# Optimization experiments

Measured on AMD Instinct MI355X. Metric: run time of the kernel, lower is better.

## Reference

```python
import jax, jax.numpy as jnp
import numpy as np

B, S, C = 8, 2048, 1024

def setup_inputs() -> dict:
    key = jax.random.key(0)
    ks = jax.random.split(key, 9)
    scale = 1.0 / np.sqrt(C)
    return {
        "x1": jax.random.normal(ks[0], (B, S, C), jnp.float32),
        "x2": jax.random.normal(ks[1], (B, S, C), jnp.float32),
        "x3": jax.random.normal(ks[2], (B, S, C), jnp.float32),
        "Wq": jax.random.normal(ks[3], (C, C), jnp.float32) * scale,
        "bq": jax.random.normal(ks[4], (C,), jnp.float32) * scale,
        "Wk": jax.random.normal(ks[5], (C, C), jnp.float32) * scale,
        "bk": jax.random.normal(ks[6], (C,), jnp.float32) * scale,
        "Wv": jax.random.normal(ks[7], (C, C), jnp.float32) * scale,
        "bv": jax.random.normal(ks[8], (C,), jnp.float32) * scale,
    }

def reference(x1, x2, x3, Wq, bq, Wk, bk, Wv, bv):
    # Linear layers: x @ W^T + b (torch nn.Linear convention, W is [out, in])
    q = jnp.einsum('bsc,dc->bsd', x1, Wq) + bq  # [B,S,C]
    k = jnp.einsum('bsc,dc->bsd', x2, Wk) + bk
    v = jnp.einsum('bsc,dc->bsd', x3, Wv) + bv
    # NOTE: original has NO 1/sqrt(d) scaling
    scores = jnp.einsum('bqd,bkd->bqk', q, k)   # [B,S,S]
    attn = jax.nn.softmax(scores, axis=-1)
    return jnp.einsum('bqk,bkd->bqd', attn, v)  # [B,S,C]
```

## Files before the change

kernel.cpp:

```cpp
#include <hip/hip_runtime.h>
#include <stdint.h>

namespace {

constexpr int Bn = 8;
constexpr int Sn = 2048;
constexpr int Cn = 1024;
constexpr int Mn = Bn * Sn;

typedef float f32x4 __attribute__((ext_vector_type(4)));
typedef _Float16 f16x8 __attribute__((ext_vector_type(8)));
typedef unsigned short us8 __attribute__((ext_vector_type(8)));

__device__ __forceinline__ unsigned short f2h(float f) {
  _Float16 h = (_Float16)f;
  unsigned short u;
  __builtin_memcpy(&u, &h, 2);
  return u;
}

__device__ __forceinline__ void stage16(const unsigned short* g, unsigned short* l) {
  __builtin_amdgcn_global_load_lds(
      (const __attribute__((address_space(1))) void*)g,
      (__attribute__((address_space(3))) void*)l, 16, 0, 0);
}

__global__ __launch_bounds__(256) void k_cast16(const float* __restrict__ src,
                                                unsigned short* __restrict__ dst, int n) {
  int stride = gridDim.x * blockDim.x;
  for (int i = blockIdx.x * blockDim.x + threadIdx.x; i * 4 < n; i += stride) {
    int j = i * 4;
    float4 v = *(const float4*)(src + j);
    ushort4 h;
    h.x = f2h(v.x); h.y = f2h(v.y); h.z = f2h(v.z); h.w = f2h(v.w);
    *(ushort4*)(dst + j) = h;
  }
}

__global__ __launch_bounds__(256) void k_bias2(const float* __restrict__ a,
                                               const float* __restrict__ b,
                                               float* __restrict__ dst) {
  int t = threadIdx.x + blockIdx.x * 256;
  if (t < Cn) { dst[t] = a[t]; dst[Cn + t] = b[t]; }
}

template <int MODE>
__global__ __launch_bounds__(512, 2) void gemm8(
    const unsigned short* __restrict__ Ah, const unsigned short* __restrict__ Bh,
    const float* __restrict__ bias,
    unsigned short* __restrict__ O0, unsigned short* __restrict__ O1,
    float* __restrict__ Sout, float* __restrict__ Of) {
  __shared__ unsigned short lds[65536];

  constexpr int KT = (MODE == 2) ? 32 : 16;
  constexpr int NIk = KT / 2;

  const int bid = blockIdx.x;
  const int chunk = bid & 7;
  const int r = bid >> 3;

  int tM, tN, side = 0, zdec = 0, lda, ldb;
  const unsigned short *a0, *b0;
  if constexpr (MODE == 0) {
    int y = chunk * 16 + (r >> 2);
    int x = r & 3;
    tM = y * 256; tN = x * 256;
    side = (y >= 64);
    a0 = Ah; b0 = Bh + side * 1048576;
    lda = 1024; ldb = 1024;
  } else if constexpr (MODE == 1) {
    zdec = chunk;
    int ys = r >> 5, x = (r >> 2) & 7, y4 = r & 3;
    tM = (ys * 4 + y4) * 256; tN = x * 256;
    a0 = Ah + (long long)zdec * 2097152;
    b0 = Bh + (long long)zdec * 2097152;
    lda = 1024; ldb = 1024;
  } else if constexpr (MODE == 2) {
    zdec = chunk;
    int y = r >> 2, x = r & 3;
    tM = y * 256; tN = x * 256;
    a0 = Ah + (long long)zdec * 8388608;
    b0 = Bh + (long long)zdec * 2048;
    lda = 4096; ldb = 16384;
  } else {
    int x = chunk * 8 + (r >> 2);
    int y = r & 3;
    tN = x * 256; tM = y * 256;
    a0 = Ah; b0 = Bh;
    lda = 1024; ldb = 1024;
  }

  const int tid = threadIdx.x;
  const int l = tid & 63;
  const int w = tid >> 6;
  const int wm = w >> 2, wn = w & 3;
  const int lr = l & 15;
  const int lk = l >> 4;
  const int ssw = ((tid & 3) ^ ((tid >> 3) & 3)) * 8;
  const int rsw = (lk ^ ((lr >> 1) & 3)) * 8;

  auto stg = [&](int region, int tile, int ks, bool isA) {
    int tt = tile < KT ? tile : KT - 1;
    int k0 = tt * 64 + ks * 32;
    const unsigned short* G = isA ? a0 : b0;
    const long long ld = isA ? lda : ldb;
    int tb = isA ? tM : tN;
    unsigned short* D = lds + region * 8192;
#pragma unroll
    for (int j = 0; j < 2; ++j)
      stage16(G + (long long)(tb + j * 128 + (tid >> 2)) * ld + k0 + ssw,
              D + j * 4096 + (size_t)tid * 8);
  };

  f32x4 acc[8][4] = {};

  stg(0, 0, 0, true);  stg(2, 0, 0, false);
  stg(1, 0, 1, true);  stg(3, 0, 1, false);
  stg(4, 1, 0, true);  stg(6, 1, 0, false);
  asm volatile("s_waitcnt vmcnt(4)" ::: "memory");
  __builtin_amdgcn_sched_barrier(0);
  __builtin_amdgcn_s_barrier();

  for (int i = 0; i < NIk; ++i) {
    const int e = 2 * i;
#pragma unroll
    for (int p = 0; p < 8; ++p) {
      const int buf = p >> 2, q = p & 3, mh = q & 1, ks = q >> 1;
      const unsigned short* Ar = lds + (buf * 4 + ks) * 8192;
      const unsigned short* Br = lds + (buf * 4 + 2 + ks) * 8192;
      f16x8 av[4], bv[4];
#pragma unroll
      for (int fm = 0; fm < 4; ++fm)
        av[fm] = *(const f16x8*)&Ar[(wm * 128 + mh * 64 + fm * 16 + lr) * 32 + rsw];
#pragma unroll
      for (int fn = 0; fn < 4; ++fn)
        bv[fn] = *(const f16x8*)&Br[(wn * 64 + fn * 16 + lr) * 32 + rsw];
      if (p == 0)      { stg(5, e + 1, 1, true); stg(7, e + 1, 1, false); }
      else if (p == 2) { stg(0, e + 2, 0, true); stg(2, e + 2, 0, false); }
      else if (p == 4) { stg(1, e + 2, 1, true); stg(3, e + 2, 1, false); }
      else if (p == 6) { stg(4, e + 3, 0, true); stg(6, e + 3, 0, false); }
      __builtin_amdgcn_s_barrier();
      asm volatile("s_waitcnt lgkmcnt(0)" ::: "memory");
      __builtin_amdgcn_sched_barrier(0);
      __builtin_amdgcn_s_setprio(1);
#pragma unroll
      for (int fm = 0; fm < 4; ++fm)
#pragma unroll
        for (int fn = 0; fn < 4; ++fn)
          acc[mh * 4 + fm][fn] = __builtin_amdgcn_mfma_f32_16x16x32_f16(
              av[fm], bv[fn], acc[mh * 4 + fm][fn], 0, 0, 0);
      __builtin_amdgcn_s_setprio(0);
      if (p == 3 || p == 7) {
        asm volatile("s_waitcnt vmcnt(4)" ::: "memory");
        __builtin_amdgcn_sched_barrier(0);
      }
      __builtin_amdgcn_s_barrier();
    }
  }

#pragma unroll
  for (int am = 0; am < 8; ++am)
#pragma unroll
    for (int an = 0; an < 4; ++an)
#pragma unroll
      for (int r2 = 0; r2 < 4; ++r2) {
        int rg = tM + wm * 128 + am * 16 + (l >> 4) * 4 + r2;
        int cg = tN + wn * 64 + an * 16 + lr;
        float v = acc[am][an][r2];
        if constexpr (MODE == 0) {
          v += bias[side * 1024 + cg];
          if (!side) {
            O0[(long long)rg * 1024 + cg] = f2h(v);
          } else {
            O1[(long long)(rg - Mn) * 1024 + cg] = f2h(v);
          }
        } else if constexpr (MODE == 1) {
          Sout[(long long)zdec * 4194304ll + (long long)rg * 2048 + cg] = v;
        } else if constexpr (MODE == 2) {
          Of[(long long)zdec * 2097152ll + (long long)rg * 1024 + cg] = v;
        } else {
          O0[(long long)rg * 16384 + cg] = f2h(v + bias[rg]);
        }
      }
}

__global__ __launch_bounds__(256) void k_softmax(float* __restrict__ S) {
  const long long row = blockIdx.x;
  float* src = S + row * Sn;
  const int t = threadIdx.x;
  float4 v0 = *(const float4*)(src + t * 8);
  float4 v1 = *(const float4*)(src + t * 8 + 4);
  float m = fmaxf(fmaxf(fmaxf(v0.x, v0.y), fmaxf(v0.z, v0.w)),
                  fmaxf(fmaxf(v1.x, v1.y), fmaxf(v1.z, v1.w)));
#pragma unroll
  for (int off = 32; off > 0; off >>= 1) m = fmaxf(m, __shfl_xor(m, off));
  __shared__ float red[8];
  if ((t & 63) == 0) red[t >> 6] = m;
  __syncthreads();
  m = fmaxf(fmaxf(red[0], red[1]), fmaxf(red[2], red[3]));
  float e[8];
  e[0] = __expf(v0.x - m); e[1] = __expf(v0.y - m);
  e[2] = __expf(v0.z - m); e[3] = __expf(v0.w - m);
  e[4] = __expf(v1.x - m); e[5] = __expf(v1.y - m);
  e[6] = __expf(v1.z - m); e[7] = __expf(v1.w - m);
  float s = ((e[0] + e[1]) + (e[2] + e[3])) + ((e[4] + e[5]) + (e[6] + e[7]));
#pragma unroll
  for (int off = 32; off > 0; off >>= 1) s += __shfl_xor(s, off);
  if ((t & 63) == 0) red[4 + (t >> 6)] = s;
  __syncthreads();
  s = (red[4] + red[5]) + (red[6] + red[7]);
  float inv = 1.0f / s;
  us8 o;
#pragma unroll
  for (int j = 0; j < 8; ++j) o[j] = f2h(e[j] * inv);
  *(us8*)((unsigned short*)src + t * 8) = o;
}

}

extern "C" void kernel_launch(void* const* d_in, const int* in_sizes, int n_in,
                              void* d_out, int out_size, void* d_ws, size_t ws_size,
                              hipStream_t stream) {
  (void)in_sizes; (void)n_in; (void)out_size;
  const float* x1 = (const float*)d_in[0];
  const float* x2 = (const float*)d_in[1];
  const float* x3 = (const float*)d_in[2];
  const float* Wq = (const float*)d_in[3];
  const float* bq = (const float*)d_in[4];
  const float* Wk = (const float*)d_in[5];
  const float* bk = (const float*)d_in[6];
  const float* Wv = (const float*)d_in[7];
  const float* bv = (const float*)d_in[8];
  float* out = (float*)d_out;
  char* ws = (char*)d_ws;

  const size_t MiB = 1048576ull;
  unsigned short* wqk = (unsigned short*)(ws);
  float* bias_cat = (float*)(ws + 4 * MiB);
  unsigned short* wvh = (unsigned short*)(ws + 5 * MiB);
  unsigned short* kh  = (unsigned short*)(ws + 12 * MiB);
  unsigned short* vT  = (unsigned short*)(ws + 44 * MiB);
  unsigned short* x3h = (unsigned short*)(ws + 76 * MiB);
  unsigned short* x1h = (unsigned short*)(ws + 76 * MiB);
  unsigned short* x2h = (unsigned short*)(ws + 108 * MiB);
  float* S = (float*)(ws + 76 * MiB);
  if (ws_size < 204 * MiB) return;

  unsigned short* qh = (unsigned short*)d_out;

  const int nx = Mn * Cn, nw = Cn * Cn;
  k_cast16<<<2048, 256, 0, stream>>>(x3, x3h, nx);
  k_cast16<<<256, 256, 0, stream>>>(Wv, wvh, nw);
  gemm8<3><<<256, 512, 0, stream>>>(wvh, x3h, bv, vT, nullptr, nullptr, nullptr);
  k_cast16<<<2048, 256, 0, stream>>>(x1, x1h, nx);
  k_cast16<<<2048, 256, 0, stream>>>(x2, x2h, nx);
  k_cast16<<<256, 256, 0, stream>>>(Wq, wqk, nw);
  k_cast16<<<256, 256, 0, stream>>>(Wk, wqk + 1048576, nw);
  k_bias2<<<4, 256, 0, stream>>>(bq, bk, bias_cat);
  gemm8<0><<<512, 512, 0, stream>>>(x1h, wqk, bias_cat, qh, kh, nullptr, nullptr);
  gemm8<1><<<512, 512, 0, stream>>>(qh, kh, nullptr, nullptr, nullptr, S, nullptr);
  k_softmax<<<Mn, 256, 0, stream>>>(S);
  gemm8<2><<<256, 512, 0, stream>>>((unsigned short*)S, vT, nullptr, nullptr,
                                    nullptr, nullptr, out);
}
```

Baseline: 369.4 us.

## Fuse all input casts into one kernel and merge Q/K/V projections into one GEMM

Replaces the seven separate fp16 cast kernels and the bias-copy kernel with a single grid-stride prep kernel that converts x1/x2/x3 and all three weights and copies the biases. The V projection (previously its own launch computing V transposed) is folded into the Q/K projection GEMM as a third 'side', so one 768-block launch produces Q, K and V^T. The softmax row mapping is also permuted across batches. This cuts launch count and per-kernel tail and idle time, at the cost of per-element divide/select overhead in the prep loop and a more branchy GEMM epilogue.

```diff
diff --git a/kernel.cpp b/kernel.cpp
--- a/kernel.cpp
+++ b/kernel.cpp
@@ -25,23 +25,40 @@
       (__attribute__((address_space(3))) void*)l, 16, 0, 0);
 }
 
-__global__ __launch_bounds__(256) void k_cast16(const float* __restrict__ src,
-                                                unsigned short* __restrict__ dst, int n) {
-  int stride = gridDim.x * blockDim.x;
-  for (int i = blockIdx.x * blockDim.x + threadIdx.x; i * 4 < n; i += stride) {
-    int j = i * 4;
-    float4 v = *(const float4*)(src + j);
+__global__ __launch_bounds__(256) void k_prep(
+    const float* __restrict__ x1, const float* __restrict__ x2,
+    const float* __restrict__ x3, const float* __restrict__ Wq,
+    const float* __restrict__ Wk, const float* __restrict__ Wv,
+    const float* __restrict__ bq, const float* __restrict__ bk,
+    const float* __restrict__ bv, unsigned short* __restrict__ xdst,
+    unsigned short* __restrict__ wdst, float* __restrict__ bdst) {
+  const int NX = 4194304;
+  const int NW = 262144;
+  int tid0 = blockIdx.x * 256 + threadIdx.x;
+  int stride = gridDim.x * 256;
+  for (int i = tid0; i < 3 * NX + 3 * NW; i += stride) {
+    const float* s;
+    unsigned short* d;
+    if (i < 3 * NX) {
+      int a = i / NX, j = i - a * NX;
+      s = (a == 0 ? x1 : a == 1 ? x2 : x3) + (size_t)j * 4;
+      d = xdst + (size_t)a * 16777216 + (size_t)j * 4;
+    } else {
+      int k = i - 3 * NX;
+      int a = k / NW, j = k - a * NW;
+      s = (a == 0 ? Wq : a == 1 ? Wk : Wv) + (size_t)j * 4;
+      d = wdst + (size_t)a * 1048576 + (size_t)j * 4;
+    }
+    float4 v = *(const float4*)s;
     ushort4 h;
     h.x = f2h(v.x); h.y = f2h(v.y); h.z = f2h(v.z); h.w = f2h(v.w);
-    *(ushort4*)(dst + j) = h;
-  }
-}
-
-__global__ __launch_bounds__(256) void k_bias2(const float* __restrict__ a,
-                                               const float* __restrict__ b,
-                                               float* __restrict__ dst) {
-  int t = threadIdx.x + blockIdx.x * 256;
-  if (t < Cn) { dst[t] = a[t]; dst[Cn + t] = b[t]; }
+    *(ushort4*)d = h;
+  }
+  if (tid0 < 768) {
+    int a = tid0 >> 8, j = tid0 & 255;
+    const float* s = (a == 0 ? bq : a == 1 ? bk : bv) + j * 4;
+    *(float4*)(bdst + a * 1024 + j * 4) = *(const float4*)s;
+  }
 }
 
 template <int MODE>
@@ -49,6 +66,7 @@
     const unsigned short* __restrict__ Ah, const unsigned short* __restrict__ Bh,
     const float* __restrict__ bias,
     unsigned short* __restrict__ O0, unsigned short* __restrict__ O1,
+    unsigned short* __restrict__ O2,
     float* __restrict__ Sout, float* __restrict__ Of) {
   __shared__ unsigned short lds[65536];
 
@@ -62,11 +80,16 @@
   int tM, tN, side = 0, zdec = 0, lda, ldb;
   const unsigned short *a0, *b0;
   if constexpr (MODE == 0) {
-    int y = chunk * 16 + (r >> 2);
+    int y = chunk * 24 + (r >> 2);
     int x = r & 3;
-    tM = y * 256; tN = x * 256;
-    side = (y >= 64);
-    a0 = Ah; b0 = Bh + side * 1048576;
+    side = (y >= 128) ? 2 : (y >= 64 ? 1 : 0);
+    if (side < 2) {
+      tM = y * 256; tN = x * 256;
+      a0 = Ah; b0 = Bh + side * 1048576;
+    } else {
+      tM = x * 256; tN = 32768 + (y - 128) * 256;
+      a0 = Bh + 2097152; b0 = Ah;
+    }
     lda = 1024; ldb = 1024;
   } else if constexpr (MODE == 1) {
     zdec = chunk;
@@ -75,19 +98,13 @@
     a0 = Ah + (long long)zdec * 2097152;
     b0 = Bh + (long long)zdec * 2097152;
     lda = 1024; ldb = 1024;
-  } else if constexpr (MODE == 2) {
+  } else {
     zdec = chunk;
     int y = r >> 2, x = r & 3;
     tM = y * 256; tN = x * 256;
     a0 = Ah + (long long)zdec * 8388608;
     b0 = Bh + (long long)zdec * 2048;
     lda = 4096; ldb = 16384;
-  } else {
-    int x = chunk * 8 + (r >> 2);
-    int y = r & 3;
-    tN = x * 256; tM = y * 256;
-    a0 = Ah; b0 = Bh;
-    lda = 1024; ldb = 1024;
   }
 
   const int tid = threadIdx.x;
@@ -168,24 +185,23 @@
         int cg = tN + wn * 64 + an * 16 + lr;
         float v = acc[am][an][r2];
         if constexpr (MODE == 0) {
-          v += bias[side * 1024 + cg];
-          if (!side) {
-            O0[(long long)rg * 1024 + cg] = f2h(v);
+          if (side == 0) {
+            O0[(long long)rg * 1024 + cg] = f2h(v + bias[cg]);
+          } else if (side == 1) {
+            O1[(long long)(rg - Mn) * 1024 + cg] = f2h(v + bias[1024 + cg]);
           } else {
-            O1[(long long)(rg - Mn) * 1024 + cg] = f2h(v);
+            O2[(long long)rg * 16384 + (cg - 32768)] = f2h(v + bias[2048 + rg]);
           }
         } else if constexpr (MODE == 1) {
           Sout[(long long)zdec * 4194304ll + (long long)rg * 2048 + cg] = v;
-        } else if constexpr (MODE == 2) {
+        } else {
           Of[(long long)zdec * 2097152ll + (long long)rg * 1024 + cg] = v;
-        } else {
-          O0[(long long)rg * 16384 + cg] = f2h(v + bias[rg]);
         }
       }
 }
 
 __global__ __launch_bounds__(256) void k_softmax(float* __restrict__ S) {
-  const long long row = blockIdx.x;
+  const long long row = ((long long)(blockIdx.x & 7) << 11) | (blockIdx.x >> 3);
   float* src = S + row * Sn;
   const int t = threadIdx.x;
   float4 v0 = *(const float4*)(src + t * 8);
@@ -236,30 +252,22 @@
 
   const size_t MiB = 1048576ull;
   unsigned short* wqk = (unsigned short*)(ws);
-  float* bias_cat = (float*)(ws + 4 * MiB);
-  unsigned short* wvh = (unsigned short*)(ws + 5 * MiB);
+  float* bias_cat = (float*)(ws + 6 * MiB);
   unsigned short* kh  = (unsigned short*)(ws + 12 * MiB);
   unsigned short* vT  = (unsigned short*)(ws + 44 * MiB);
-  unsigned short* x3h = (unsigned short*)(ws + 76 * MiB);
   unsigned short* x1h = (unsigned short*)(ws + 76 * MiB);
-  unsigned short* x2h = (unsigned short*)(ws + 108 * MiB);
   float* S = (float*)(ws + 76 * MiB);
   if (ws_size < 204 * MiB) return;
 
   unsigned short* qh = (unsigned short*)d_out;
 
-  const int nx = Mn * Cn, nw = Cn * Cn;
-  k_cast16<<<2048, 256, 0, stream>>>(x3, x3h, nx);
-  k_cast16<<<256, 256, 0, stream>>>(Wv, wvh, nw);
-  gemm8<3><<<256, 512, 0, stream>>>(wvh, x3h, bv, vT, nullptr, nullptr, nullptr);
-  k_cast16<<<2048, 256, 0, stream>>>(x1, x1h, nx);
-  k_cast16<<<2048, 256, 0, stream>>>(x2, x2h, nx);
-  k_cast16<<<256, 256, 0, stream>>>(Wq, wqk, nw);
-  k_cast16<<<256, 256, 0, stream>>>(Wk, wqk + 1048576, nw);
-  k_bias2<<<4, 256, 0, stream>>>(bq, bk, bias_cat);
-  gemm8<0><<<512, 512, 0, stream>>>(x1h, wqk, bias_cat, qh, kh, nullptr, nullptr);
-  gemm8<1><<<512, 512, 0, stream>>>(qh, kh, nullptr, nullptr, nullptr, S, nullptr);
+  k_prep<<<2048, 256, 0, stream>>>(x1, x2, x3, Wq, Wk, Wv, bq, bk, bv,
+                                   x1h, wqk, bias_cat);
+  gemm8<0><<<768, 512, 0, stream>>>(x1h, wqk, bias_cat, qh, kh, vT,
+                                    nullptr, nullptr);
+  gemm8<1><<<512, 512, 0, stream>>>(qh, kh, nullptr, nullptr, nullptr, nullptr,
+                                    S, nullptr);
   k_softmax<<<Mn, 256, 0, stream>>>(S);
   gemm8<2><<<256, 512, 0, stream>>>((unsigned short*)S, vT, nullptr, nullptr,
-                                    nullptr, nullptr, out);
-}
+                                    nullptr, nullptr, nullptr, out);
+}
```

After: 383.6 us. 1.04x slower.
